# Optimization experiments

Hardware: AMD Instinct MI355X
Metric: run time of the kernel (lower is better)

## Reference

```python
import jax, jax.numpy as jnp
import numpy as np

EMBED_DIM = 1024
NUM_HEADS = 16
HEAD_DIM = EMBED_DIM // NUM_HEADS


def setup_inputs() -> dict:
    key = jax.random.key(0)
    ks = jax.random.split(key, 7)
    B, N, C = 2, 2048, EMBED_DIM
    s = 1.0 / np.sqrt(C)
    return {
        "x": jax.random.normal(ks[0], (B, N, C), dtype=jnp.float32),
        "phase_signal": jax.random.uniform(ks[1], (B,), dtype=jnp.float32),
        "qkv_w": jax.random.normal(ks[2], (3 * C, C), dtype=jnp.float32) * s,
        "qkv_b": jnp.zeros((3 * C,), dtype=jnp.float32),
        "proj_w": jax.random.normal(ks[3], (C, C), dtype=jnp.float32) * s,
        "proj_b": jnp.zeros((C,), dtype=jnp.float32),
        "phase_weight": jnp.ones((NUM_HEADS,), dtype=jnp.float32),
    }


def reference(x, phase_signal, qkv_w, qkv_b, proj_w, proj_b, phase_weight):
    B, N, C = x.shape
    H, D = NUM_HEADS, HEAD_DIM
    # qkv projection: [B,N,3C] -> [3,B,H,N,D]
    qkv = (x @ qkv_w.T + qkv_b).reshape(B, N, 3, H, D)
    qkv = jnp.transpose(qkv, (2, 0, 3, 1, 4))
    q, k, v = qkv[0], qkv[1], qkv[2]
    attn = jnp.einsum("bhnd,bhmd->bhnm", q, k) * (D ** -0.5)
    # per-(batch, head) phase modulation applied before softmax
    phase_mod = phase_weight[None, :, None, None] * phase_signal[:, None, None, None]
    attn = attn * (1.0 + 0.2 * phase_mod)
    attn = jax.nn.softmax(attn, axis=-1)  # dropout is identity in eval mode
    out = jnp.einsum("bhnm,bhmd->bhnd", attn, v)
    out = jnp.transpose(out, (0, 2, 1, 3)).reshape(B, N, C)
    return out @ proj_w.T + proj_b
```

## Files before the change

kernel.cpp:

```cpp
#include <hip/hip_runtime.h>
#include <stdint.h>

#define NUM_H 16
#define HD    64
#define CDIM  1024
#define NSEQ  2048
#define NBATCH 2
#define LOG2E 1.4426950408889634f

typedef __attribute__((ext_vector_type(8))) short short8;
typedef __attribute__((ext_vector_type(4))) float f32x4;
typedef __attribute__((ext_vector_type(16))) float f32x16;
typedef __attribute__((ext_vector_type(4))) unsigned short ushort4v;
typedef __attribute__((ext_vector_type(4))) float float4v;
typedef __attribute__((ext_vector_type(2))) unsigned int u32x2;

__device__ __forceinline__ unsigned short f2bf(float f) {
    unsigned int u = __builtin_bit_cast(unsigned int, f);
    unsigned int r = u + 0x7fffu + ((u >> 16) & 1u);
    return (unsigned short)(r >> 16);
}

__device__ __forceinline__ unsigned int cvtpk(float a, float b) {
    unsigned int r;
    asm("v_cvt_pk_bf16_f32 %0, %1, %2" : "=v"(r) : "v"(a), "v"(b));
    return r;
}

__device__ __forceinline__ void plswap(unsigned int &a, unsigned int &b) {
    asm("v_permlane32_swap_b32 %0, %1" : "+v"(a), "+v"(b));
}

__device__ __forceinline__ void gload_lds16(const void* g, const void* l) {
    __builtin_amdgcn_global_load_lds(
        (const __attribute__((address_space(1))) unsigned int*)(unsigned long long)(uintptr_t)g,
        (__attribute__((address_space(3))) unsigned int*)(unsigned int)(uintptr_t)l,
        16, 0, 0);
}

__global__ void cvt_bf16_kernel(const float* __restrict__ in,
                                unsigned short* __restrict__ out, int n4) {
    int i = blockIdx.x * blockDim.x + threadIdx.x;
    if (i < n4) {
        float4v v = *(const float4v*)(in + (size_t)i * 4);
        ushort4v o;
        o[0] = f2bf(v[0]); o[1] = f2bf(v[1]); o[2] = f2bf(v[2]); o[3] = f2bf(v[3]);
        *(ushort4v*)(out + (size_t)i * 4) = o;
    }
}

__global__ __launch_bounds__(256, 2) void gemm_qkv(
    const unsigned short* __restrict__ A,
    const unsigned short* __restrict__ Bw,
    const float* __restrict__ bias,
    const float* __restrict__ ps,
    const float* __restrict__ pw,
    unsigned short* __restrict__ qb,
    unsigned short* __restrict__ kb,
    unsigned short* __restrict__ vtb)
{
    __shared__ unsigned short As[2][128 * 64];
    __shared__ unsigned short Bs[2][128 * 64];
    const int tid = threadIdx.x;
    const int wid = tid >> 6;
    const int lane = tid & 63;
    const int l15 = lane & 15, l4 = lane >> 4;

    const int bid = blockIdx.y * 32 + blockIdx.x;
    const int wg = (bid & 7) * 96 + (bid >> 3);
    const int bm = wg & 31, bn = wg >> 5;
    const int wr = wid >> 1, wc = wid & 1;

    f32x4 acc[4][4];
    const f32x4 zero4 = {0.f, 0.f, 0.f, 0.f};
#pragma unroll
    for (int m = 0; m < 4; ++m)
#pragma unroll
        for (int n = 0; n < 4; ++n) acc[m][n] = zero4;

    const int jr = lane >> 3;
    const int jc = ((lane & 7) ^ jr) << 4;
    const char* aB = (const char*)A  + (size_t)(bm * 128) * 2048;
    const char* bB = (const char*)Bw + (size_t)(bn * 128) * 2048;

    auto stage = [&](int buf, int k0) {
#pragma unroll
        for (int i = 0; i < 4; ++i) {
            const int rowb = wid * 32 + i * 8;
            gload_lds16(aB + (size_t)(rowb + jr) * 2048 + k0 * 2 + jc,
                        (const char*)&As[buf][0] + rowb * 128);
            gload_lds16(bB + (size_t)(rowb + jr) * 2048 + k0 * 2 + jc,
                        (const char*)&Bs[buf][0] + rowb * 128);
        }
    };

    const int swz = (l15 & 7) << 4;

    stage(0, 0);
    for (int it = 0; it < 16; ++it) {
        const int buf = it & 1;
        __syncthreads();
        if (it < 15) stage(buf ^ 1, (it + 1) * 64);
#pragma unroll
        for (int kk = 0; kk < 2; ++kk) {
            short8 a[4], b[4];
#pragma unroll
            for (int m = 0; m < 4; ++m)
                a[m] = *(const short8*)((const char*)&As[buf][0] +
                        (wr * 64 + m * 16 + l15) * 128 + ((kk * 64 + l4 * 16) ^ swz));
#pragma unroll
            for (int n = 0; n < 4; ++n)
                b[n] = *(const short8*)((const char*)&Bs[buf][0] +
                        (wc * 64 + n * 16 + l15) * 128 + ((kk * 64 + l4 * 16) ^ swz));
            __builtin_amdgcn_s_setprio(1);
#pragma unroll
            for (int m = 0; m < 4; ++m)
#pragma unroll
                for (int n = 0; n < 4; ++n)
                    acc[m][n] = __builtin_amdgcn_mfma_f32_16x16x32_bf16(a[m], b[n], acc[m][n], 0, 0, 0);
            __builtin_amdgcn_s_setprio(0);
        }
    }

    const int row_base = bm * 128 + wr * 64;
    const int col_base = bn * 128 + wc * 64;
    const float ps0 = ps[0], ps1 = ps[1];
#pragma unroll
    for (int n = 0; n < 4; ++n) {
        const int col3 = col_base + n * 16 + l15;
        const float bv = bias[col3];
        const int t3 = col3 >> 10;
        const int hh = (col3 >> 6) & 15;
        const int dd = col3 & 63;
        float kf0 = 1.f, kf1 = 1.f;
        if (t3 == 1) {
            const float base = 0.125f * LOG2E;
            const float pwh = pw[hh];
            kf0 = base * (1.f + 0.2f * pwh * ps0);
            kf1 = base * (1.f + 0.2f * pwh * ps1);
        }
#pragma unroll
        for (int m = 0; m < 4; ++m) {
#pragma unroll
            for (int r = 0; r < 4; ++r) {
                const int row = row_base + m * 16 + l4 * 4 + r;
                const int bb = row >> 11, nn = row & 2047;
                const size_t bh = (size_t)(bb * 16 + hh);
                if (t3 == 0) {
                    qb[(bh * 2048 + nn) * 64 + dd] = f2bf(acc[m][n][r] + bv);
                } else if (t3 == 1) {
                    const float kf = (bb == 0) ? kf0 : kf1;
                    kb[(bh * 2048 + nn) * 64 + dd] = f2bf((acc[m][n][r] + bv) * kf);
                } else {
                    vtb[(bh * 64 + dd) * 2048 + nn] = f2bf(acc[m][n][r] + bv);
                }
            }
        }
    }
}

__global__ __launch_bounds__(256, 2) void gemm_proj(
    const unsigned short* __restrict__ A,
    const unsigned short* __restrict__ Bw,
    const float* __restrict__ bias,
    float* __restrict__ out)
{
    __shared__ unsigned short As[2][128 * 64];
    __shared__ unsigned short Bs[2][128 * 64];
    const int tid = threadIdx.x;
    const int wid = tid >> 6;
    const int lane = tid & 63;
    const int l15 = lane & 15, l4 = lane >> 4;

    const int bid = blockIdx.y * 32 + blockIdx.x;
    const int wg = (bid & 7) * 32 + (bid >> 3);
    const int bm = wg & 31, bn = wg >> 5;
    const int wr = wid >> 1, wc = wid & 1;

    f32x4 acc[4][4];
    const f32x4 zero4 = {0.f, 0.f, 0.f, 0.f};
#pragma unroll
    for (int m = 0; m < 4; ++m)
#pragma unroll
        for (int n = 0; n < 4; ++n) acc[m][n] = zero4;

    const int jr = lane >> 3;
    const int jc = ((lane & 7) ^ jr) << 4;
    const char* aB = (const char*)A  + (size_t)(bm * 128) * 2048;
    const char* bB = (const char*)Bw + (size_t)(bn * 128) * 2048;

    auto stage = [&](int buf, int k0) {
#pragma unroll
        for (int i = 0; i < 4; ++i) {
            const int rowb = wid * 32 + i * 8;
            gload_lds16(aB + (size_t)(rowb + jr) * 2048 + k0 * 2 + jc,
                        (const char*)&As[buf][0] + rowb * 128);
            gload_lds16(bB + (size_t)(rowb + jr) * 2048 + k0 * 2 + jc,
                        (const char*)&Bs[buf][0] + rowb * 128);
        }
    };

    const int swz = (l15 & 7) << 4;

    stage(0, 0);
    for (int it = 0; it < 16; ++it) {
        const int buf = it & 1;
        __syncthreads();
        if (it < 15) stage(buf ^ 1, (it + 1) * 64);
#pragma unroll
        for (int kk = 0; kk < 2; ++kk) {
            short8 a[4], b[4];
#pragma unroll
            for (int m = 0; m < 4; ++m)
                a[m] = *(const short8*)((const char*)&As[buf][0] +
                        (wr * 64 + m * 16 + l15) * 128 + ((kk * 64 + l4 * 16) ^ swz));
#pragma unroll
            for (int n = 0; n < 4; ++n)
                b[n] = *(const short8*)((const char*)&Bs[buf][0] +
                        (wc * 64 + n * 16 + l15) * 128 + ((kk * 64 + l4 * 16) ^ swz));
            __builtin_amdgcn_s_setprio(1);
#pragma unroll
            for (int m = 0; m < 4; ++m)
#pragma unroll
                for (int n = 0; n < 4; ++n)
                    acc[m][n] = __builtin_amdgcn_mfma_f32_16x16x32_bf16(a[m], b[n], acc[m][n], 0, 0, 0);
            __builtin_amdgcn_s_setprio(0);
        }
    }

    const int row_base = bm * 128 + wr * 64;
    const int col_base = bn * 128 + wc * 64;
#pragma unroll
    for (int n = 0; n < 4; ++n) {
        const int col = col_base + n * 16 + l15;
        const float bv = bias[col];
#pragma unroll
        for (int m = 0; m < 4; ++m) {
#pragma unroll
            for (int r = 0; r < 4; ++r) {
                const int row = row_base + m * 16 + l4 * 4 + r;
                out[(size_t)row * 1024 + col] = acc[m][n][r] + bv;
            }
        }
    }
}

__global__ __launch_bounds__(256, 2) void attn_kernel(
    const unsigned short* __restrict__ qb,
    const unsigned short* __restrict__ kb,
    const unsigned short* __restrict__ vtb,
    unsigned short* __restrict__ aout)
{
    __shared__ unsigned short KVs[2][2][64 * 64];

    const int tid = threadIdx.x;
    const int w = tid >> 6;
    const int l = tid & 63;
    const int l31 = l & 31;
    const int hi = l >> 5;

    const int bid = blockIdx.y * 16 + blockIdx.x;
    const int wg = (bid & 7) * 64 + (bid >> 3);
    const int bh = wg >> 4;
    const int b = bh >> 4, h = bh & 15;
    const int q0 = (wg & 15) * 128 + w * 32;

    const char* qg = (const char*)(qb + (size_t)bh * 2048 * 64);
    const char* kg = (const char*)(kb + (size_t)bh * 2048 * 64);
    const char* vg = (const char*)(vtb + (size_t)bh * 64 * 2048);

    short8 qf[4];
#pragma unroll
    for (int t = 0; t < 4; ++t)
        qf[t] = *(const short8*)(qg + (size_t)(q0 + l31) * 128 + t * 32 + hi * 16);

    f32x16 oacc[2];
#pragma unroll
    for (int dt = 0; dt < 2; ++dt)
#pragma unroll
        for (int r = 0; r < 16; ++r) oacc[dt][r] = 0.f;
    float lr = 0.f;

    const int jr = l >> 3;
    const int jc = ((l & 7) ^ jr) << 4;
    auto stage = [&](int buf, int kv0) {
#pragma unroll
        for (int i = 0; i < 2; ++i) {
            const int row = w * 16 + i * 8;
            gload_lds16(kg + (size_t)(kv0 + row + jr) * 128 + jc,
                        (const char*)&KVs[buf][0][0] + row * 128);
            gload_lds16(vg + (size_t)(row + jr) * 4096 + (size_t)kv0 * 2 + jc,
                        (const char*)&KVs[buf][1][0] + row * 128);
        }
    };

    stage(0, 0);
    __syncthreads();

    const int swz = (l31 & 7) << 4;

    for (int it = 0; it < 32; ++it) {
        const int buf = it & 1;
        if (it < 31) stage(buf ^ 1, (it + 1) * 64);

        const char* Kb = (const char*)&KVs[buf][0][0];
        const char* Vb = (const char*)&KVs[buf][1][0];

        f32x16 sa[2];
        __builtin_amdgcn_s_setprio(1);
#pragma unroll
        for (int s = 0; s < 2; ++s) {
#pragma unroll
            for (int r = 0; r < 16; ++r) sa[s][r] = 0.f;
#pragma unroll
            for (int t = 0; t < 4; ++t) {
                const short8 kf = *(const short8*)(Kb + (s * 32 + l31) * 128 +
                                                   ((t * 32 + hi * 16) ^ swz));
                sa[s] = __builtin_amdgcn_mfma_f32_32x32x16_bf16(kf, qf[t], sa[s], 0, 0, 0);
            }
        }
        __builtin_amdgcn_s_setprio(0);

#pragma unroll
        for (int s = 0; s < 2; ++s)
#pragma unroll
            for (int r = 0; r < 16; ++r)
                sa[s][r] = __builtin_amdgcn_exp2f(sa[s][r] - 20.0f);

        float ts[16];
#pragma unroll
        for (int r = 0; r < 16; ++r) ts[r] = sa[0][r] + sa[1][r];
#pragma unroll
        for (int d = 8; d >= 1; d >>= 1)
#pragma unroll
            for (int r = 0; r < 8; ++r)
                if (r < d) ts[r] += ts[r + d];
        lr += ts[0] + __shfl_xor(ts[0], 32);

#pragma unroll
        for (int s = 0; s < 2; ++s) {
            unsigned int wv[8];
#pragma unroll
            for (int g = 0; g < 8; ++g)
                wv[g] = cvtpk(sa[s][g * 2], sa[s][g * 2 + 1]);
            plswap(wv[0], wv[2]); plswap(wv[1], wv[3]);
            plswap(wv[4], wv[6]); plswap(wv[5], wv[7]);
            union { unsigned int u[4]; short8 s8; } f0, f1;
            f0.u[0] = wv[0]; f0.u[1] = wv[1]; f0.u[2] = wv[2]; f0.u[3] = wv[3];
            f1.u[0] = wv[4]; f1.u[1] = wv[5]; f1.u[2] = wv[6]; f1.u[3] = wv[7];
            __builtin_amdgcn_s_setprio(1);
#pragma unroll
            for (int dt = 0; dt < 2; ++dt) {
                const short8 v0 = *(const short8*)(Vb + (dt * 32 + l31) * 128 +
                                                   (((s * 2 + 0) * 32 + hi * 16) ^ swz));
                oacc[dt] = __builtin_amdgcn_mfma_f32_32x32x16_bf16(v0, f0.s8, oacc[dt], 0, 0, 0);
                const short8 v1 = *(const short8*)(Vb + (dt * 32 + l31) * 128 +
                                                   (((s * 2 + 1) * 32 + hi * 16) ^ swz));
                oacc[dt] = __builtin_amdgcn_mfma_f32_32x32x16_bf16(v1, f1.s8, oacc[dt], 0, 0, 0);
            }
            __builtin_amdgcn_s_setprio(0);
        }
        __syncthreads();
    }

    const float inv = 1.0f / lr;
    char* outp = (char*)aout + ((size_t)(b * 2048 + q0 + l31) * 1024 + h * 64) * 2;
#pragma unroll
    for (int dt = 0; dt < 2; ++dt)
#pragma unroll
        for (int rg = 0; rg < 4; ++rg) {
            u32x2 pkd;
            pkd[0] = cvtpk(oacc[dt][rg * 4 + 0] * inv, oacc[dt][rg * 4 + 1] * inv);
            pkd[1] = cvtpk(oacc[dt][rg * 4 + 2] * inv, oacc[dt][rg * 4 + 3] * inv);
            *(u32x2*)(outp + (size_t)(dt * 32 + rg * 8 + hi * 4) * 2) = pkd;
        }
}

extern "C" void kernel_launch(void* const* d_in, const int* in_sizes, int n_in,
                              void* d_out, int out_size, void* d_ws, size_t ws_size,
                              hipStream_t stream) {
    const float* x      = (const float*)d_in[0];
    const float* ps     = (const float*)d_in[1];
    const float* qkv_w  = (const float*)d_in[2];
    const float* qkv_b  = (const float*)d_in[3];
    const float* proj_w = (const float*)d_in[4];
    const float* proj_b = (const float*)d_in[5];
    const float* pw     = (const float*)d_in[6];
    float* out = (float*)d_out;
    char* ws = (char*)d_ws;

    unsigned short* x_bf    = (unsigned short*)(ws);
    unsigned short* w1_bf   = (unsigned short*)(ws + (8u  << 20));
    unsigned short* wp_bf   = (unsigned short*)(ws + (14u << 20));
    unsigned short* qb      = (unsigned short*)(ws + (16u << 20));
    unsigned short* kb      = (unsigned short*)(ws + (24u << 20));
    unsigned short* vtb     = (unsigned short*)(ws + (32u << 20));
    unsigned short* attn_bf = x_bf;

    cvt_bf16_kernel<<<4096, 256, 0, stream>>>(x,      x_bf,  1048576);
    cvt_bf16_kernel<<<3072, 256, 0, stream>>>(qkv_w,  w1_bf, 786432);
    cvt_bf16_kernel<<<1024, 256, 0, stream>>>(proj_w, wp_bf, 262144);

    gemm_qkv<<<dim3(32, 24), 256, 0, stream>>>(x_bf, w1_bf, qkv_b, ps, pw, qb, kb, vtb);
    attn_kernel<<<dim3(16, 32), 256, 0, stream>>>(qb, kb, vtb, attn_bf);
    gemm_proj<<<dim3(32, 8), 256, 0, stream>>>(attn_bf, wp_bf, proj_b, out);
}
```

Baseline: 126.6 us.

## Restructure QKV GEMM into 256x256 tiles with 8-wave ping-pong pipeline

The QKV projection GEMM moves from 128x128 tiles with 4 waves to 256x256 tiles with 8 waves. Each wave computes 128x64 in four quadrant phases, separated by barriers, and loads for tile t+2 are interleaved between MFMA phases across half-tile LDS buffers. The aim is to raise arithmetic intensity and overlap global loads with MFMA work. In exchange the grid shrinks to 192 blocks, fewer than there are CUs, and the XCD-aware block remapping is dropped from both GEMMs.

```diff
diff --git a/kernel.cpp b/kernel.cpp
--- a/kernel.cpp
+++ b/kernel.cpp
@@ -49,7 +49,7 @@
     }
 }
 
-__global__ __launch_bounds__(256, 2) void gemm_qkv(
+__global__ __launch_bounds__(512, 2) void gemm_qkv(
     const unsigned short* __restrict__ A,
     const unsigned short* __restrict__ Bw,
     const float* __restrict__ bias,
@@ -59,71 +59,138 @@
     unsigned short* __restrict__ kb,
     unsigned short* __restrict__ vtb)
 {
-    __shared__ unsigned short As[2][128 * 64];
-    __shared__ unsigned short Bs[2][128 * 64];
+    __shared__ unsigned short lds[2][2][2][128][64];
+
     const int tid = threadIdx.x;
     const int wid = tid >> 6;
     const int lane = tid & 63;
     const int l15 = lane & 15, l4 = lane >> 4;
-
-    const int bid = blockIdx.y * 32 + blockIdx.x;
-    const int wg = (bid & 7) * 96 + (bid >> 3);
-    const int bm = wg & 31, bn = wg >> 5;
-    const int wr = wid >> 1, wc = wid & 1;
-
-    f32x4 acc[4][4];
+    const int wave_m = wid >> 2, wave_n = wid & 3;
+
+    const int bm = blockIdx.x;
+    const int bn = blockIdx.y;
+
+    f32x4 acc[8][4];
     const f32x4 zero4 = {0.f, 0.f, 0.f, 0.f};
 #pragma unroll
-    for (int m = 0; m < 4; ++m)
+    for (int m = 0; m < 8; ++m)
 #pragma unroll
         for (int n = 0; n < 4; ++n) acc[m][n] = zero4;
 
     const int jr = lane >> 3;
     const int jc = ((lane & 7) ^ jr) << 4;
-    const char* aB = (const char*)A  + (size_t)(bm * 128) * 2048;
-    const char* bB = (const char*)Bw + (size_t)(bn * 128) * 2048;
-
-    auto stage = [&](int buf, int k0) {
-#pragma unroll
-        for (int i = 0; i < 4; ++i) {
-            const int rowb = wid * 32 + i * 8;
-            gload_lds16(aB + (size_t)(rowb + jr) * 2048 + k0 * 2 + jc,
-                        (const char*)&As[buf][0] + rowb * 128);
-            gload_lds16(bB + (size_t)(rowb + jr) * 2048 + k0 * 2 + jc,
-                        (const char*)&Bs[buf][0] + rowb * 128);
-        }
+    const char* aB = (const char*)A  + (size_t)(bm * 256) * 2048;
+    const char* bB = (const char*)Bw + (size_t)(bn * 256) * 2048;
+
+    auto stageH = [&](int t, int which) {
+        const int buf = t & 1;
+        const int op = which >> 1, hf = which & 1;
+        const char* src = (op == 0) ? aB : bB;
+        const int rowb = hf * 128 + wid * 16;
+        const size_t k0b = (size_t)t * 128;
+        char* dst = (char*)&lds[buf][op][hf][wid * 16][0];
+#pragma unroll
+        for (int i = 0; i < 2; ++i)
+            gload_lds16(src + (size_t)(rowb + i * 8 + jr) * 2048 + k0b + jc,
+                        dst + i * 1024);
     };
 
     const int swz = (l15 & 7) << 4;
-
-    stage(0, 0);
-    for (int it = 0; it < 16; ++it) {
-        const int buf = it & 1;
-        __syncthreads();
-        if (it < 15) stage(buf ^ 1, (it + 1) * 64);
-#pragma unroll
-        for (int kk = 0; kk < 2; ++kk) {
-            short8 a[4], b[4];
-#pragma unroll
-            for (int m = 0; m < 4; ++m)
-                a[m] = *(const short8*)((const char*)&As[buf][0] +
-                        (wr * 64 + m * 16 + l15) * 128 + ((kk * 64 + l4 * 16) ^ swz));
-#pragma unroll
-            for (int n = 0; n < 4; ++n)
-                b[n] = *(const short8*)((const char*)&Bs[buf][0] +
-                        (wc * 64 + n * 16 + l15) * 128 + ((kk * 64 + l4 * 16) ^ swz));
-            __builtin_amdgcn_s_setprio(1);
-#pragma unroll
-            for (int m = 0; m < 4; ++m)
-#pragma unroll
-                for (int n = 0; n < 4; ++n)
-                    acc[m][n] = __builtin_amdgcn_mfma_f32_16x16x32_bf16(a[m], b[n], acc[m][n], 0, 0, 0);
-            __builtin_amdgcn_s_setprio(0);
-        }
-    }
-
-    const int row_base = bm * 128 + wr * 64;
-    const int col_base = bn * 128 + wc * 64;
+    auto rdA = [&](int buf, int mq, int mp, int kk) -> short8 {
+        return *(const short8*)((const char*)&lds[buf][0][wave_m][mq * 64 + mp * 16 + l15][0]
+                                + ((kk * 64 + l4 * 16) ^ swz));
+    };
+    auto rdB = [&](int buf, int nq, int np, int kk) -> short8 {
+        const int br = wave_n * 64 + nq * 32 + np * 16 + l15;
+        return *(const short8*)((const char*)&lds[buf][1][br >> 7][br & 127][0]
+                                + ((kk * 64 + l4 * 16) ^ swz));
+    };
+
+    stageH(0, 0); stageH(0, 1); stageH(0, 2); stageH(0, 3);
+    stageH(1, 2); stageH(1, 3); stageH(1, 0); stageH(1, 1);
+    asm volatile("s_waitcnt vmcnt(8)" ::: "memory");
+    __builtin_amdgcn_s_barrier();
+
+    for (int t = 0; t < 16; ++t) {
+        const int buf = t & 1;
+        short8 af[4][2], bf[2][2][2];
+
+#pragma unroll
+        for (int mp = 0; mp < 4; ++mp) {
+            af[mp][0] = rdA(buf, 0, mp, 0); af[mp][1] = rdA(buf, 0, mp, 1);
+        }
+#pragma unroll
+        for (int np = 0; np < 2; ++np) {
+            bf[0][np][0] = rdB(buf, 0, np, 0); bf[0][np][1] = rdB(buf, 0, np, 1);
+        }
+        __builtin_amdgcn_s_barrier();
+        __builtin_amdgcn_s_setprio(1);
+#pragma unroll
+        for (int mp = 0; mp < 4; ++mp)
+#pragma unroll
+            for (int np = 0; np < 2; ++np)
+#pragma unroll
+                for (int kk = 0; kk < 2; ++kk)
+                    acc[mp][np] = __builtin_amdgcn_mfma_f32_16x16x32_bf16(
+                        af[mp][kk], bf[0][np][kk], acc[mp][np], 0, 0, 0);
+        __builtin_amdgcn_s_setprio(0);
+        __builtin_amdgcn_s_barrier();
+
+#pragma unroll
+        for (int np = 0; np < 2; ++np) {
+            bf[1][np][0] = rdB(buf, 1, np, 0); bf[1][np][1] = rdB(buf, 1, np, 1);
+        }
+        if (t < 14) stageH(t + 2, 2);
+        __builtin_amdgcn_s_barrier();
+        __builtin_amdgcn_s_setprio(1);
+#pragma unroll
+        for (int mp = 0; mp < 4; ++mp)
+#pragma unroll
+            for (int np = 0; np < 2; ++np)
+#pragma unroll
+                for (int kk = 0; kk < 2; ++kk)
+                    acc[mp][2 + np] = __builtin_amdgcn_mfma_f32_16x16x32_bf16(
+                        af[mp][kk], bf[1][np][kk], acc[mp][2 + np], 0, 0, 0);
+        __builtin_amdgcn_s_setprio(0);
+        __builtin_amdgcn_s_barrier();
+
+#pragma unroll
+        for (int mp = 0; mp < 4; ++mp) {
+            af[mp][0] = rdA(buf, 1, mp, 0); af[mp][1] = rdA(buf, 1, mp, 1);
+        }
+        if (t < 14) stageH(t + 2, 3);
+        __builtin_amdgcn_s_barrier();
+        __builtin_amdgcn_s_setprio(1);
+#pragma unroll
+        for (int mp = 0; mp < 4; ++mp)
+#pragma unroll
+            for (int np = 0; np < 2; ++np)
+#pragma unroll
+                for (int kk = 0; kk < 2; ++kk)
+                    acc[4 + mp][np] = __builtin_amdgcn_mfma_f32_16x16x32_bf16(
+                        af[mp][kk], bf[0][np][kk], acc[4 + mp][np], 0, 0, 0);
+        __builtin_amdgcn_s_setprio(0);
+        __builtin_amdgcn_s_barrier();
+
+        if (t < 14) { stageH(t + 2, 0); stageH(t + 2, 1); }
+        __builtin_amdgcn_s_barrier();
+        __builtin_amdgcn_s_setprio(1);
+#pragma unroll
+        for (int mp = 0; mp < 4; ++mp)
+#pragma unroll
+            for (int np = 0; np < 2; ++np)
+#pragma unroll
+                for (int kk = 0; kk < 2; ++kk)
+                    acc[4 + mp][2 + np] = __builtin_amdgcn_mfma_f32_16x16x32_bf16(
+                        af[mp][kk], bf[1][np][kk], acc[4 + mp][2 + np], 0, 0, 0);
+        __builtin_amdgcn_s_setprio(0);
+        if (t < 14)       { asm volatile("s_waitcnt vmcnt(8)" ::: "memory"); }
+        else if (t == 14) { asm volatile("s_waitcnt vmcnt(0)" ::: "memory"); }
+        __builtin_amdgcn_s_barrier();
+    }
+
+    const int row_base = bm * 256 + wave_m * 128;
+    const int col_base = bn * 256 + wave_n * 64;
     const float ps0 = ps[0], ps1 = ps[1];
 #pragma unroll
     for (int n = 0; n < 4; ++n) {
@@ -140,7 +207,7 @@
             kf1 = base * (1.f + 0.2f * pwh * ps1);
         }
 #pragma unroll
-        for (int m = 0; m < 4; ++m) {
+        for (int m = 0; m < 8; ++m) {
 #pragma unroll
             for (int r = 0; r < 4; ++r) {
                 const int row = row_base + m * 16 + l4 * 4 + r;
@@ -171,10 +238,7 @@
     const int wid = tid >> 6;
     const int lane = tid & 63;
     const int l15 = lane & 15, l4 = lane >> 4;
-
-    const int bid = blockIdx.y * 32 + blockIdx.x;
-    const int wg = (bid & 7) * 32 + (bid >> 3);
-    const int bm = wg & 31, bn = wg >> 5;
+    const int bm = blockIdx.x, bn = blockIdx.y;
     const int wr = wid >> 1, wc = wid & 1;
 
     f32x4 acc[4][4];
@@ -401,7 +465,7 @@
     cvt_bf16_kernel<<<3072, 256, 0, stream>>>(qkv_w,  w1_bf, 786432);
     cvt_bf16_kernel<<<1024, 256, 0, stream>>>(proj_w, wp_bf, 262144);
 
-    gemm_qkv<<<dim3(32, 24), 256, 0, stream>>>(x_bf, w1_bf, qkv_b, ps, pw, qb, kb, vtb);
+    gemm_qkv<<<dim3(16, 12), 512, 0, stream>>>(x_bf, w1_bf, qkv_b, ps, pw, qb, kb, vtb);
     attn_kernel<<<dim3(16, 32), 256, 0, stream>>>(qb, kb, vtb, attn_bf);
     gemm_proj<<<dim3(32, 8), 256, 0, stream>>>(attn_bf, wp_bf, proj_b, out);
 }
```

Result: slower. 133.9 us (+5.8%).
